# Kernel tuning notes

Measured on AMD Instinct MI355X. Metric: run time of the kernel, lower is better.

Reference implementation:

```python
import jax, jax.numpy as jnp
import numpy as np

D_MODEL = 1024
N_HEADS = 16
D_K = D_MODEL // N_HEADS
B, T = 2, 2048
EPS = 1e-6


def _phi(x):
    # elu(x) + 1
    return jax.nn.elu(x) + 1.0


def setup_inputs() -> dict:
    key = jax.random.key(0)
    ks = jax.random.split(key, 5)
    s = 1.0 / np.sqrt(D_MODEL)
    return {
        "x": jax.random.normal(ks[0], (B, T, D_MODEL), jnp.float32),
        "Wq": jax.random.normal(ks[1], (D_MODEL, D_MODEL), jnp.float32) * s,
        "bq": jnp.zeros((D_MODEL,), jnp.float32),
        "Wk": jax.random.normal(ks[2], (D_MODEL, D_MODEL), jnp.float32) * s,
        "bk": jnp.zeros((D_MODEL,), jnp.float32),
        "Wv": jax.random.normal(ks[3], (D_MODEL, D_MODEL), jnp.float32) * s,
        "bv": jnp.zeros((D_MODEL,), jnp.float32),
        "Wo": jax.random.normal(ks[4], (D_MODEL, D_MODEL), jnp.float32) * s,
        "bo": jnp.zeros((D_MODEL,), jnp.float32),
    }


def reference(x, Wq, bq, Wk, bk, Wv, bv, Wo, bo):
    Bv_, Tv_, _ = x.shape
    # projections (torch nn.Linear: x @ W.T + b), split heads -> [B, H, T, d_k]
    def proj(W, b):
        y = x @ W.T + b
        return y.reshape(Bv_, Tv_, N_HEADS, D_K).transpose(0, 2, 1, 3)

    q = _phi(proj(Wq, bq))
    k = _phi(proj(Wk, bk))
    v = proj(Wv, bv)

    # causal linear attention: running kv outer-product and k prefix sums
    kv = jnp.einsum("bhtd,bhte->bhtde", k, v)          # [B,H,T,d_k,d_k]
    kv = jnp.cumsum(kv, axis=2)
    k_cum = jnp.cumsum(k, axis=2)
    out = jnp.einsum("bhtd,bhtde->bhte", q, kv)        # [B,H,T,d_k]
    z = jnp.einsum("bhtd,bhtd->bht", q, k_cum)         # [B,H,T]
    out = out / (z[..., None] + EPS)

    out = out.transpose(0, 2, 1, 3).reshape(Bv_, Tv_, N_HEADS * D_K)
    return out @ Wo.T + bo
```

## Files before the change

kernel.cpp:

```cpp
#include <hip/hip_runtime.h>


typedef float  f32x4   __attribute__((ext_vector_type(4)));
typedef __bf16 bf16x8  __attribute__((ext_vector_type(8)));
typedef short  short8v __attribute__((ext_vector_type(8)));
typedef short  short4v __attribute__((ext_vector_type(4)));

static __device__ __forceinline__ short f2bf(float f) {
    unsigned u = __float_as_uint(f);
    u += 0x7FFFu + ((u >> 16) & 1u);
    return (short)(u >> 16);
}
static __device__ __forceinline__ float bf2f(short s) {
    return __uint_as_float(((unsigned)(unsigned short)s) << 16);
}
static __device__ __forceinline__ float phi(float x) {
    return x > 0.f ? x + 1.f : __expf(x);
}
static __device__ __forceinline__ void gl_lds16(const short* g, short* l) {
    __builtin_amdgcn_global_load_lds(
        (const __attribute__((address_space(1))) void*)g,
        (__attribute__((address_space(3))) void*)l, 16, 0, 0);
}

#define LDT 72
static __device__ __forceinline__ int swz(int row, int col) {
    return row * LDT + (col ^ (row & 56));
}

__global__ __launch_bounds__(256) void convert_bf16(
    const float* __restrict__ x,  const float* __restrict__ Wq,
    const float* __restrict__ Wk, const float* __restrict__ Wv,
    const float* __restrict__ Wo,
    short* __restrict__ xb,  short* __restrict__ Wqb,
    short* __restrict__ Wkb, short* __restrict__ Wvb, short* __restrict__ Wob)
{
    const int blk = blockIdx.x;
    const float* src; short* dst; size_t base;
    if (blk < 2048)      { src = x;  dst = xb;  base = (size_t)blk * 2048; }
    else if (blk < 2560) { src = Wq; dst = Wqb; base = (size_t)(blk - 2048) * 2048; }
    else if (blk < 3072) { src = Wk; dst = Wkb; base = (size_t)(blk - 2560) * 2048; }
    else if (blk < 3584) { src = Wv; dst = Wvb; base = (size_t)(blk - 3072) * 2048; }
    else                 { src = Wo; dst = Wob; base = (size_t)(blk - 3584) * 2048; }
    const size_t o = base + (size_t)threadIdx.x * 8;
    f32x4 v0 = *(const f32x4*)&src[o];
    f32x4 v1 = *(const f32x4*)&src[o + 4];
    short8v s;
#pragma unroll
    for (int m = 0; m < 4; ++m) { s[m] = f2bf(v0[m]); s[m + 4] = f2bf(v1[m]); }
    *(short8v*)&dst[o] = s;
}

__global__ __launch_bounds__(256) void gemm_qkv(
    const short* __restrict__ xb,
    const short* __restrict__ Wqb, const short* __restrict__ Wkb,
    const short* __restrict__ Wvb,
    const float* __restrict__ bq, const float* __restrict__ bk,
    const float* __restrict__ bv,
    short* __restrict__ Qb, short* __restrict__ Kb, short* __restrict__ Vb)
{
    __shared__ short As[2][128 * 32];
    __shared__ short Bs[2][128 * 32];
    const int tid = threadIdx.x;
    const int bm = blockIdx.x, bn = blockIdx.y;
    const int wsel = bn >> 3;
    const int n0 = (bn & 7) << 7;
    const short* __restrict__ W    = (wsel == 0) ? Wqb : (wsel == 1) ? Wkb : Wvb;
    const float* __restrict__ bias = (wsel == 0) ? bq  : (wsel == 1) ? bk  : bv;
    short* __restrict__ Ob         = (wsel == 0) ? Qb  : (wsel == 1) ? Kb  : Vb;
    const int m0 = bm << 7;
    const int wave = tid >> 6, lane = tid & 63;
    const int wm = (wave & 1) << 6, wn = (wave >> 1) << 6;
    const int l15 = lane & 15, quad = lane >> 4;

    const int ch0 = wave * 2, ch1 = ch0 + 1;
    const int lrow = lane >> 2;
    const int lcol = (((lane & 3) ^ ((lane >> 3) & 3)) << 3);
    const short* ga0 = xb + (size_t)(m0 + ch0 * 16 + lrow) * 1024 + lcol;
    const short* ga1 = xb + (size_t)(m0 + ch1 * 16 + lrow) * 1024 + lcol;
    const short* gb0 = W  + (size_t)(n0 + ch0 * 16 + lrow) * 1024 + lcol;
    const short* gb1 = W  + (size_t)(n0 + ch1 * 16 + lrow) * 1024 + lcol;
    short* la0[2] = { &As[0][ch0 * 512], &As[1][ch0 * 512] };
    short* la1[2] = { &As[0][ch1 * 512], &As[1][ch1 * 512] };
    short* lb0[2] = { &Bs[0][ch0 * 512], &Bs[1][ch0 * 512] };
    short* lb1[2] = { &Bs[0][ch1 * 512], &Bs[1][ch1 * 512] };

    const int rslot = (quad ^ ((l15 >> 1) & 3)) << 3;

#define QKV_STAGE(K, BUF)                    \
    do {                                     \
        gl_lds16(ga0 + (K), la0[BUF]);       \
        gl_lds16(ga1 + (K), la1[BUF]);       \
        gl_lds16(gb0 + (K), lb0[BUF]);       \
        gl_lds16(gb1 + (K), lb1[BUF]);       \
    } while (0)

#define QKV_COMPUTE(BUF)                                                              \
    do {                                                                              \
        bf16x8 a[4], b[4];                                                            \
        _Pragma("unroll")                                                             \
        for (int i = 0; i < 4; ++i)                                                   \
            a[i] = *(const bf16x8*)&As[BUF][(wm + i * 16 + l15) * 32 + rslot];        \
        _Pragma("unroll")                                                             \
        for (int j = 0; j < 4; ++j)                                                   \
            b[j] = *(const bf16x8*)&Bs[BUF][(wn + j * 16 + l15) * 32 + rslot];        \
        _Pragma("unroll")                                                             \
        for (int i = 0; i < 4; ++i)                                                   \
            _Pragma("unroll")                                                         \
            for (int j = 0; j < 4; ++j)                                               \
                acc[i][j] = __builtin_amdgcn_mfma_f32_16x16x32_bf16(a[i], b[j],       \
                                                                   acc[i][j], 0, 0, 0); \
    } while (0)

    f32x4 acc[4][4] = {};
    QKV_STAGE(0, 0);
    for (int k0 = 0; k0 < 1024; k0 += 64) {
        asm volatile("s_waitcnt vmcnt(0)" ::: "memory");
        __syncthreads();
        QKV_STAGE(k0 + 32, 1);
        QKV_COMPUTE(0);
        asm volatile("s_waitcnt vmcnt(0)" ::: "memory");
        __syncthreads();
        if (k0 + 64 < 1024) QKV_STAGE(k0 + 64, 0);
        QKV_COMPUTE(1);
    }
#undef QKV_STAGE
#undef QKV_COMPUTE

#pragma unroll
    for (int i = 0; i < 4; ++i)
#pragma unroll
        for (int j = 0; j < 4; ++j) {
            const int col = n0 + wn + j * 16 + l15;
            const int h = col >> 6, d = col & 63;
            const float bv_ = bias[col];
            const int row0 = m0 + wm + i * 16 + quad * 4;
            const int b = row0 >> 11, t0 = row0 & 2047;
            const size_t obase = ((size_t)(b * 16 + h) * 2048 + t0) * 64 + d;
#pragma unroll
            for (int r = 0; r < 4; ++r) {
                float v = acc[i][j][r] + bv_;
                if (wsel < 2) v = phi(v);
                Ob[obase + (size_t)r * 64] = f2bf(v);
            }
        }
}

__global__ __launch_bounds__(256) void chunk_sums(
    const short* __restrict__ Kb, const short* __restrict__ Vb,
    short* __restrict__ KVsum, float* __restrict__ ksum)
{
    __shared__ short KT[64 * LDT];
    __shared__ short VT[64 * LDT];
    __shared__ float pS[256];
    const int c = blockIdx.x, bh = blockIdx.y;
    const int tid = threadIdx.x;
    const int w = tid >> 6, lane = tid & 63, l15 = lane & 15, quad = lane >> 4;
    const size_t tilebase = ((size_t)bh * 2048 + c * 64) * 64;

#pragma unroll
    for (int p = 0; p < 2; ++p) {
        const int t = (tid >> 3) + p * 32;
        const int e0 = (tid & 7) << 3;
        const size_t g = tilebase + (size_t)t * 64 + e0;
        short8v kv = *(const short8v*)&Kb[g];
        short8v vv = *(const short8v*)&Vb[g];
#pragma unroll
        for (int jj = 0; jj < 8; ++jj) {
            KT[swz(e0 + jj, t)] = kv[jj];
            VT[swz(e0 + jj, t)] = vv[jj];
        }
    }
    __syncthreads();

    f32x4 acc[4] = {};
#pragma unroll
    for (int k0 = 0; k0 < 64; k0 += 32) {
        const int ra = w * 16 + l15;
        bf16x8 a = *(const bf16x8*)&KT[ra * LDT + ((k0 + quad * 8) ^ (ra & 56))];
#pragma unroll
        for (int tj = 0; tj < 4; ++tj) {
            const int rb = tj * 16 + l15;
            bf16x8 bfr = *(const bf16x8*)&VT[rb * LDT + ((k0 + quad * 8) ^ (rb & 56))];
            acc[tj] = __builtin_amdgcn_mfma_f32_16x16x32_bf16(a, bfr, acc[tj], 0, 0, 0);
        }
    }
    short* __restrict__ outp = KVsum + (((size_t)bh * 32) + c) * 4096;
#pragma unroll
    for (int tj = 0; tj < 4; ++tj)
#pragma unroll
        for (int r = 0; r < 4; ++r)
            outp[(w * 16 + quad * 4 + r) * 64 + tj * 16 + l15] = f2bf(acc[tj][r]);

    {
        const int d = tid & 63, part = tid >> 6;
        short8v k1 = *(const short8v*)&KT[d * LDT + ((part * 16) ^ (d & 56))];
        short8v k2 = *(const short8v*)&KT[d * LDT + ((part * 16 + 8) ^ (d & 56))];
        float s = 0.f;
#pragma unroll
        for (int m = 0; m < 8; ++m) s += bf2f(k1[m]) + bf2f(k2[m]);
        pS[part * 64 + d] = s;
    }
    __syncthreads();
    if (tid < 64)
        ksum[(((size_t)bh * 32) + c) * 64 + tid] =
            pS[tid] + pS[tid + 64] + pS[tid + 128] + pS[tid + 192];
}

__global__ __launch_bounds__(256) void scan_chunks(
    const short* __restrict__ KVsum, const float* __restrict__ ksum,
    short* __restrict__ KVpref, float* __restrict__ kpref)
{
    const int bh = blockIdx.y;
    const int o = blockIdx.x * 256 + threadIdx.x;
    const size_t base = (size_t)bh * 32 * 4096 + o;
    short v[32];
#pragma unroll
    for (int cc = 0; cc < 32; ++cc) v[cc] = KVsum[base + (size_t)cc * 4096];
    float run = 0.f;
#pragma unroll
    for (int cc = 0; cc < 32; ++cc) {
        KVpref[base + (size_t)cc * 4096] = f2bf(run);
        run += bf2f(v[cc]);
    }
    if (blockIdx.x == 0 && threadIdx.x < 64) {
        float vals[32];
        const size_t kb = (size_t)bh * 32 * 64 + threadIdx.x;
#pragma unroll
        for (int cc = 0; cc < 32; ++cc) vals[cc] = ksum[kb + (size_t)cc * 64];
        float r2 = 0.f;
#pragma unroll
        for (int cc = 0; cc < 32; ++cc) { kpref[kb + (size_t)cc * 64] = r2; r2 += vals[cc]; }
    }
}

__global__ __launch_bounds__(256) void attn_chunk(
    const short* __restrict__ Qb, const short* __restrict__ Kb,
    const short* __restrict__ Vb, const short* __restrict__ KVpref,
    const float* __restrict__ kpref, short* __restrict__ attnb)
{
    __shared__ short Qs[64 * LDT];
    __shared__ short KS[64 * LDT];
    __shared__ short VT[64 * LDT];
    __shared__ short KVT[64 * LDT];
    const int c = blockIdx.x, bh = blockIdx.y;
    const int b = bh >> 4, h = bh & 15;
    const int tid = threadIdx.x;
    const int w = tid >> 6, lane = tid & 63, l15 = lane & 15, quad = lane >> 4;
    const size_t tilebase = ((size_t)bh * 2048 + c * 64) * 64;
    const short* __restrict__ KVc = KVpref + (((size_t)bh * 32) + c) * 4096;

#pragma unroll
    for (int p = 0; p < 2; ++p) {
        const int t = (tid >> 3) + p * 32;
        const int e0 = (tid & 7) << 3;
        const size_t g = tilebase + (size_t)t * 64 + e0;
        *(short8v*)&Qs[t * LDT + e0] = *(const short8v*)&Qb[g];
        *(short8v*)&KS[t * LDT + e0] = *(const short8v*)&Kb[g];
        short8v vv = *(const short8v*)&Vb[g];
        short8v pv = *(const short8v*)&KVc[t * 64 + e0];
#pragma unroll
        for (int jj = 0; jj < 8; ++jj) {
            VT[swz(e0 + jj, t)]  = vv[jj];
            KVT[swz(e0 + jj, t)] = pv[jj];
        }
    }
    __syncthreads();

    f32x4 sacc[4] = {};
#pragma unroll
    for (int k0 = 0; k0 < 64; k0 += 32) {
        bf16x8 a = *(const bf16x8*)&Qs[(w * 16 + l15) * LDT + k0 + quad * 8];
#pragma unroll
        for (int tj = 0; tj < 4; ++tj) {
            bf16x8 bfr = *(const bf16x8*)&KS[(tj * 16 + l15) * LDT + k0 + quad * 8];
            sacc[tj] = __builtin_amdgcn_mfma_f32_16x16x32_bf16(a, bfr, sacc[tj], 0, 0, 0);
        }
    }

    f32x4 kp4 = *(const f32x4*)&kpref[(((size_t)bh * 32) + c) * 64 + l15 * 4];
    float zinv[4];
#pragma unroll
    for (int r = 0; r < 4; ++r) {
        const int i = w * 16 + quad * 4 + r;
        float p = 0.f;
#pragma unroll
        for (int tj = 0; tj < 4; ++tj)
            if (tj * 16 + l15 <= i) p += sacc[tj][r];
        short4v q4 = *(const short4v*)&Qs[i * LDT + l15 * 4];
#pragma unroll
        for (int m = 0; m < 4; ++m) p += bf2f(q4[m]) * kp4[m];
        p += __shfl_xor(p, 1);
        p += __shfl_xor(p, 2);
        p += __shfl_xor(p, 4);
        p += __shfl_xor(p, 8);
        zinv[r] = 1.f / (p + 1e-6f);
    }

    __syncthreads();
#pragma unroll
    for (int tj = 0; tj < 4; ++tj)
#pragma unroll
        for (int r = 0; r < 4; ++r) {
            const int i = w * 16 + quad * 4 + r;
            const int j = tj * 16 + l15;
            KS[i * LDT + j] = f2bf(j <= i ? sacc[tj][r] : 0.f);
        }

    f32x4 oacc[4] = {};
#pragma unroll
    for (int k0 = 0; k0 < 64; k0 += 32) {
        bf16x8 a1 = *(const bf16x8*)&KS[(w * 16 + l15) * LDT + k0 + quad * 8];
        bf16x8 a2 = *(const bf16x8*)&Qs[(w * 16 + l15) * LDT + k0 + quad * 8];
#pragma unroll
        for (int tj = 0; tj < 4; ++tj) {
            const int rb = tj * 16 + l15;
            bf16x8 b1 = *(const bf16x8*)&VT[rb * LDT + ((k0 + quad * 8) ^ (rb & 56))];
            bf16x8 b2 = *(const bf16x8*)&KVT[rb * LDT + ((k0 + quad * 8) ^ (rb & 56))];
            oacc[tj] = __builtin_amdgcn_mfma_f32_16x16x32_bf16(a1, b1, oacc[tj], 0, 0, 0);
            oacc[tj] = __builtin_amdgcn_mfma_f32_16x16x32_bf16(a2, b2, oacc[tj], 0, 0, 0);
        }
    }
    const size_t arowbase = (size_t)b * 2048 + c * 64;
#pragma unroll
    for (int tj = 0; tj < 4; ++tj)
#pragma unroll
        for (int r = 0; r < 4; ++r) {
            const int i = w * 16 + quad * 4 + r;
            const int e = tj * 16 + l15;
            attnb[(arowbase + i) * 1024 + h * 64 + e] = f2bf(oacc[tj][r] * zinv[r]);
        }
}

__global__ __launch_bounds__(256) void gemm_out(
    const short* __restrict__ attnb, const short* __restrict__ Wob,
    const float* __restrict__ bo, float* __restrict__ outp)
{
    __shared__ short As[2][128 * 32];
    __shared__ short Bs[2][64 * 32];
    const int tid = threadIdx.x;
    const int bm = blockIdx.x, bn = blockIdx.y;
    const int m0 = bm << 7, n0 = bn << 6;
    const int wave = tid >> 6, lane = tid & 63;
    const int wm = (wave & 1) << 6, wn = (wave >> 1) << 5;
    const int l15 = lane & 15, quad = lane >> 4;

    const int lrow = lane >> 2;
    const int lcol = (((lane & 3) ^ ((lane >> 3) & 3)) << 3);
    const short* gp[3]; short* lp[2][3];
#pragma unroll
    for (int cc = 0; cc < 3; ++cc) {
        const int ch = wave * 3 + cc;
        if (ch < 8) {
            gp[cc] = attnb + (size_t)(m0 + ch * 16 + lrow) * 1024 + lcol;
            lp[0][cc] = &As[0][ch * 512];
            lp[1][cc] = &As[1][ch * 512];
        } else {
            gp[cc] = Wob + (size_t)(n0 + (ch - 8) * 16 + lrow) * 1024 + lcol;
            lp[0][cc] = &Bs[0][(ch - 8) * 512];
            lp[1][cc] = &Bs[1][(ch - 8) * 512];
        }
    }
    const int rslot = (quad ^ ((l15 >> 1) & 3)) << 3;

#define OUT_STAGE(K, BUF)                     \
    do {                                      \
        gl_lds16(gp[0] + (K), lp[BUF][0]);    \
        gl_lds16(gp[1] + (K), lp[BUF][1]);    \
        gl_lds16(gp[2] + (K), lp[BUF][2]);    \
    } while (0)

#define OUT_COMPUTE(BUF)                                                              \
    do {                                                                              \
        bf16x8 a[4], b[2];                                                            \
        _Pragma("unroll")                                                             \
        for (int i = 0; i < 4; ++i)                                                   \
            a[i] = *(const bf16x8*)&As[BUF][(wm + i * 16 + l15) * 32 + rslot];        \
        _Pragma("unroll")                                                             \
        for (int j = 0; j < 2; ++j)                                                   \
            b[j] = *(const bf16x8*)&Bs[BUF][(wn + j * 16 + l15) * 32 + rslot];        \
        _Pragma("unroll")                                                             \
        for (int i = 0; i < 4; ++i)                                                   \
            _Pragma("unroll")                                                         \
            for (int j = 0; j < 2; ++j)                                               \
                acc[i][j] = __builtin_amdgcn_mfma_f32_16x16x32_bf16(a[i], b[j],       \
                                                                   acc[i][j], 0, 0, 0); \
    } while (0)

    f32x4 acc[4][2] = {};
    OUT_STAGE(0, 0);
    for (int k0 = 0; k0 < 1024; k0 += 64) {
        asm volatile("s_waitcnt vmcnt(0)" ::: "memory");
        __syncthreads();
        OUT_STAGE(k0 + 32, 1);
        OUT_COMPUTE(0);
        asm volatile("s_waitcnt vmcnt(0)" ::: "memory");
        __syncthreads();
        if (k0 + 64 < 1024) OUT_STAGE(k0 + 64, 0);
        OUT_COMPUTE(1);
    }
#undef OUT_STAGE
#undef OUT_COMPUTE

#pragma unroll
    for (int i = 0; i < 4; ++i)
#pragma unroll
        for (int j = 0; j < 2; ++j) {
            const int col = n0 + wn + j * 16 + l15;
            const float bv_ = bo[col];
#pragma unroll
            for (int r = 0; r < 4; ++r) {
                const int row = m0 + wm + i * 16 + quad * 4 + r;
                outp[(size_t)row * 1024 + col] = acc[i][j][r] + bv_;
            }
        }
}

extern "C" void kernel_launch(void* const* d_in, const int* in_sizes, int n_in,
                              void* d_out, int out_size, void* d_ws, size_t ws_size,
                              hipStream_t stream)
{
    const float* x  = (const float*)d_in[0];
    const float* Wq = (const float*)d_in[1];
    const float* bq = (const float*)d_in[2];
    const float* Wk = (const float*)d_in[3];
    const float* bk = (const float*)d_in[4];
    const float* Wv = (const float*)d_in[5];
    const float* bv = (const float*)d_in[6];
    const float* Wo = (const float*)d_in[7];
    const float* bo = (const float*)d_in[8];

    char* ws = (char*)d_ws;
    short* xb     = (short*)(ws + 0);
    short* Wqb    = (short*)(ws + 8388608);
    short* Wkb    = (short*)(ws + 10485760);
    short* Wvb    = (short*)(ws + 12582912);
    short* Wob    = (short*)(ws + 14680064);
    short* Qb     = (short*)(ws + 16777216);
    short* Kb     = (short*)(ws + 25165824);
    short* Vb     = (short*)(ws + 33554432);
    short* KVsum  = (short*)(ws + 41943040);
    short* KVpref = (short*)(ws + 50331648);
    short* attnb  = (short*)(ws + 58720256);
    float* ksum   = (float*)(ws + 67108864);
    float* kpref  = (float*)(ws + 67371008);
    float* outp   = (float*)d_out;

    convert_bf16<<<4096, 256, 0, stream>>>(x, Wq, Wk, Wv, Wo, xb, Wqb, Wkb, Wvb, Wob);
    gemm_qkv   <<<dim3(32, 24), 256, 0, stream>>>(xb, Wqb, Wkb, Wvb, bq, bk, bv, Qb, Kb, Vb);
    chunk_sums <<<dim3(32, 32), 256, 0, stream>>>(Kb, Vb, KVsum, ksum);
    scan_chunks<<<dim3(16, 32), 256, 0, stream>>>(KVsum, ksum, KVpref, kpref);
    attn_chunk <<<dim3(32, 32), 256, 0, stream>>>(Qb, Kb, Vb, KVpref, kpref, attnb);
    gemm_out   <<<dim3(32, 16), 256, 0, stream>>>(attnb, Wob, bo, outp);
}
```

Baseline: 160.7 us.

## Fuse all six stages into one persistent kernel with grid barriers

```diff
diff --git a/kernel.cpp b/kernel.cpp
--- a/kernel.cpp
+++ b/kernel.cpp
@@ -28,64 +28,99 @@
     return row * LDT + (col ^ (row & 56));
 }
 
-__global__ __launch_bounds__(256) void convert_bf16(
-    const float* __restrict__ x,  const float* __restrict__ Wq,
-    const float* __restrict__ Wk, const float* __restrict__ Wv,
-    const float* __restrict__ Wo,
-    short* __restrict__ xb,  short* __restrict__ Wqb,
-    short* __restrict__ Wkb, short* __restrict__ Wvb, short* __restrict__ Wob)
+#define NBLK 768
+
+static __device__ __forceinline__ void gbar(unsigned* bar) {
+    __syncthreads();
+    if (threadIdx.x == 0) {
+        unsigned* arrive = bar;
+        unsigned* gen    = bar + 32;
+        __builtin_amdgcn_fence(__ATOMIC_RELEASE, "agent");
+        unsigned g = __hip_atomic_load(gen, __ATOMIC_RELAXED, __HIP_MEMORY_SCOPE_AGENT);
+        unsigned a = __hip_atomic_fetch_add(arrive, 1u, __ATOMIC_RELAXED, __HIP_MEMORY_SCOPE_AGENT);
+        if (a == NBLK - 1u) {
+            __hip_atomic_store(arrive, 0u, __ATOMIC_RELAXED, __HIP_MEMORY_SCOPE_AGENT);
+            __hip_atomic_store(gen, g + 1u, __ATOMIC_RELEASE, __HIP_MEMORY_SCOPE_AGENT);
+        } else {
+            while (__hip_atomic_load(gen, __ATOMIC_RELAXED, __HIP_MEMORY_SCOPE_AGENT) == g)
+                __builtin_amdgcn_s_sleep(8);
+        }
+        __builtin_amdgcn_fence(__ATOMIC_ACQUIRE, "agent");
+    }
+    __syncthreads();
+}
+
+__global__ __launch_bounds__(256, 3) void mega(
+    const float* __restrict__ x,
+    const float* __restrict__ Wq, const float* __restrict__ bq,
+    const float* __restrict__ Wk, const float* __restrict__ bk,
+    const float* __restrict__ Wv, const float* __restrict__ bv,
+    const float* __restrict__ Wo, const float* __restrict__ bo,
+    char* __restrict__ ws, float* __restrict__ outp)
 {
-    const int blk = blockIdx.x;
-    const float* src; short* dst; size_t base;
-    if (blk < 2048)      { src = x;  dst = xb;  base = (size_t)blk * 2048; }
-    else if (blk < 2560) { src = Wq; dst = Wqb; base = (size_t)(blk - 2048) * 2048; }
-    else if (blk < 3072) { src = Wk; dst = Wkb; base = (size_t)(blk - 2560) * 2048; }
-    else if (blk < 3584) { src = Wv; dst = Wvb; base = (size_t)(blk - 3072) * 2048; }
-    else                 { src = Wo; dst = Wob; base = (size_t)(blk - 3584) * 2048; }
-    const size_t o = base + (size_t)threadIdx.x * 8;
-    f32x4 v0 = *(const f32x4*)&src[o];
-    f32x4 v1 = *(const f32x4*)&src[o + 4];
-    short8v s;
-#pragma unroll
-    for (int m = 0; m < 4; ++m) { s[m] = f2bf(v0[m]); s[m + 4] = f2bf(v1[m]); }
-    *(short8v*)&dst[o] = s;
-}
-
-__global__ __launch_bounds__(256) void gemm_qkv(
-    const short* __restrict__ xb,
-    const short* __restrict__ Wqb, const short* __restrict__ Wkb,
-    const short* __restrict__ Wvb,
-    const float* __restrict__ bq, const float* __restrict__ bk,
-    const float* __restrict__ bv,
-    short* __restrict__ Qb, short* __restrict__ Kb, short* __restrict__ Vb)
-{
-    __shared__ short As[2][128 * 32];
-    __shared__ short Bs[2][128 * 32];
+    __shared__ __align__(16) char smem[36864];
+
+    const int bid = blockIdx.x;
     const int tid = threadIdx.x;
-    const int bm = blockIdx.x, bn = blockIdx.y;
-    const int wsel = bn >> 3;
-    const int n0 = (bn & 7) << 7;
-    const short* __restrict__ W    = (wsel == 0) ? Wqb : (wsel == 1) ? Wkb : Wvb;
-    const float* __restrict__ bias = (wsel == 0) ? bq  : (wsel == 1) ? bk  : bv;
-    short* __restrict__ Ob         = (wsel == 0) ? Qb  : (wsel == 1) ? Kb  : Vb;
-    const int m0 = bm << 7;
     const int wave = tid >> 6, lane = tid & 63;
-    const int wm = (wave & 1) << 6, wn = (wave >> 1) << 6;
     const int l15 = lane & 15, quad = lane >> 4;
 
-    const int ch0 = wave * 2, ch1 = ch0 + 1;
-    const int lrow = lane >> 2;
-    const int lcol = (((lane & 3) ^ ((lane >> 3) & 3)) << 3);
-    const short* ga0 = xb + (size_t)(m0 + ch0 * 16 + lrow) * 1024 + lcol;
-    const short* ga1 = xb + (size_t)(m0 + ch1 * 16 + lrow) * 1024 + lcol;
-    const short* gb0 = W  + (size_t)(n0 + ch0 * 16 + lrow) * 1024 + lcol;
-    const short* gb1 = W  + (size_t)(n0 + ch1 * 16 + lrow) * 1024 + lcol;
-    short* la0[2] = { &As[0][ch0 * 512], &As[1][ch0 * 512] };
-    short* la1[2] = { &As[0][ch1 * 512], &As[1][ch1 * 512] };
-    short* lb0[2] = { &Bs[0][ch0 * 512], &Bs[1][ch0 * 512] };
-    short* lb1[2] = { &Bs[0][ch1 * 512], &Bs[1][ch1 * 512] };
-
-    const int rslot = (quad ^ ((l15 >> 1) & 3)) << 3;
+    short* xb     = (short*)(ws + 0);
+    short* Wqb    = (short*)(ws + 8388608);
+    short* Wkb    = (short*)(ws + 10485760);
+    short* Wvb    = (short*)(ws + 12582912);
+    short* Wob    = (short*)(ws + 14680064);
+    short* Qb     = (short*)(ws + 16777216);
+    short* Kb     = (short*)(ws + 25165824);
+    short* Vb     = (short*)(ws + 33554432);
+    short* KVsum  = (short*)(ws + 41943040);
+    short* KVpref = (short*)(ws + 50331648);
+    short* attnb  = (short*)(ws + 58720256);
+    float* ksum   = (float*)(ws + 67108864);
+    float* kpref  = (float*)(ws + 67371008);
+    unsigned* bar = (unsigned*)(ws + 68157440);
+
+    for (int u = bid; u < 4096; u += NBLK) {
+        const float* src; short* dst; size_t base;
+        if (u < 2048)      { src = x;  dst = xb;  base = (size_t)u * 2048; }
+        else if (u < 2560) { src = Wq; dst = Wqb; base = (size_t)(u - 2048) * 2048; }
+        else if (u < 3072) { src = Wk; dst = Wkb; base = (size_t)(u - 2560) * 2048; }
+        else if (u < 3584) { src = Wv; dst = Wvb; base = (size_t)(u - 3072) * 2048; }
+        else               { src = Wo; dst = Wob; base = (size_t)(u - 3584) * 2048; }
+        const size_t o = base + (size_t)tid * 8;
+        f32x4 v0 = *(const f32x4*)&src[o];
+        f32x4 v1 = *(const f32x4*)&src[o + 4];
+        short8v s;
+#pragma unroll
+        for (int m = 0; m < 4; ++m) { s[m] = f2bf(v0[m]); s[m + 4] = f2bf(v1[m]); }
+        *(short8v*)&dst[o] = s;
+    }
+    gbar(bar);
+
+    {
+        short* Asb[2] = { (short*)smem,        (short*)smem + 4096 };
+        short* Bsb[2] = { (short*)smem + 8192, (short*)smem + 12288 };
+        const int bm = bid & 31, bn = bid >> 5;
+        const int wsel = bn >> 3;
+        const int n0 = (bn & 7) << 7;
+        const short* __restrict__ W    = (wsel == 0) ? Wqb : (wsel == 1) ? Wkb : Wvb;
+        const float* __restrict__ bias = (wsel == 0) ? bq  : (wsel == 1) ? bk  : bv;
+        short* __restrict__ Ob         = (wsel == 0) ? Qb  : (wsel == 1) ? Kb  : Vb;
+        const int m0 = bm << 7;
+        const int wm = (wave & 1) << 6, wn = (wave >> 1) << 6;
+
+        const int ch0 = wave * 2, ch1 = ch0 + 1;
+        const int lrow = lane >> 2;
+        const int lcol = (((lane & 3) ^ ((lane >> 3) & 3)) << 3);
+        const short* ga0 = xb + (size_t)(m0 + ch0 * 16 + lrow) * 1024 + lcol;
+        const short* ga1 = xb + (size_t)(m0 + ch1 * 16 + lrow) * 1024 + lcol;
+        const short* gb0 = W  + (size_t)(n0 + ch0 * 16 + lrow) * 1024 + lcol;
+        const short* gb1 = W  + (size_t)(n0 + ch1 * 16 + lrow) * 1024 + lcol;
+        short* la0[2] = { Asb[0] + ch0 * 512, Asb[1] + ch0 * 512 };
+        short* la1[2] = { Asb[0] + ch1 * 512, Asb[1] + ch1 * 512 };
+        short* lb0[2] = { Bsb[0] + ch0 * 512, Bsb[1] + ch0 * 512 };
+        short* lb1[2] = { Bsb[0] + ch1 * 512, Bsb[1] + ch1 * 512 };
+        const int rslot = (quad ^ ((l15 >> 1) & 3)) << 3;
 
 #define QKV_STAGE(K, BUF)                    \
     do {                                     \
@@ -94,16 +129,15 @@
         gl_lds16(gb0 + (K), lb0[BUF]);       \
         gl_lds16(gb1 + (K), lb1[BUF]);       \
     } while (0)
-
 #define QKV_COMPUTE(BUF)                                                              \
     do {                                                                              \
         bf16x8 a[4], b[4];                                                            \
         _Pragma("unroll")                                                             \
         for (int i = 0; i < 4; ++i)                                                   \
-            a[i] = *(const bf16x8*)&As[BUF][(wm + i * 16 + l15) * 32 + rslot];        \
+            a[i] = *(const bf16x8*)&Asb[BUF][(wm + i * 16 + l15) * 32 + rslot];       \
         _Pragma("unroll")                                                             \
         for (int j = 0; j < 4; ++j)                                                   \
-            b[j] = *(const bf16x8*)&Bs[BUF][(wn + j * 16 + l15) * 32 + rslot];        \
+            b[j] = *(const bf16x8*)&Bsb[BUF][(wn + j * 16 + l15) * 32 + rslot];       \
         _Pragma("unroll")                                                             \
         for (int i = 0; i < 4; ++i)                                                   \
             _Pragma("unroll")                                                         \
@@ -112,256 +146,247 @@
                                                                    acc[i][j], 0, 0, 0); \
     } while (0)
 
-    f32x4 acc[4][4] = {};
-    QKV_STAGE(0, 0);
-    for (int k0 = 0; k0 < 1024; k0 += 64) {
-        asm volatile("s_waitcnt vmcnt(0)" ::: "memory");
-        __syncthreads();
-        QKV_STAGE(k0 + 32, 1);
-        QKV_COMPUTE(0);
-        asm volatile("s_waitcnt vmcnt(0)" ::: "memory");
-        __syncthreads();
-        if (k0 + 64 < 1024) QKV_STAGE(k0 + 64, 0);
-        QKV_COMPUTE(1);
-    }
+        f32x4 acc[4][4] = {};
+        QKV_STAGE(0, 0);
+        for (int k0 = 0; k0 < 1024; k0 += 64) {
+            asm volatile("s_waitcnt vmcnt(0)" ::: "memory");
+            __syncthreads();
+            QKV_STAGE(k0 + 32, 1);
+            QKV_COMPUTE(0);
+            asm volatile("s_waitcnt vmcnt(0)" ::: "memory");
+            __syncthreads();
+            if (k0 + 64 < 1024) QKV_STAGE(k0 + 64, 0);
+            QKV_COMPUTE(1);
+        }
 #undef QKV_STAGE
 #undef QKV_COMPUTE
 
 #pragma unroll
-    for (int i = 0; i < 4; ++i)
-#pragma unroll
-        for (int j = 0; j < 4; ++j) {
-            const int col = n0 + wn + j * 16 + l15;
-            const int h = col >> 6, d = col & 63;
-            const float bv_ = bias[col];
-            const int row0 = m0 + wm + i * 16 + quad * 4;
-            const int b = row0 >> 11, t0 = row0 & 2047;
-            const size_t obase = ((size_t)(b * 16 + h) * 2048 + t0) * 64 + d;
+        for (int i = 0; i < 4; ++i)
+#pragma unroll
+            for (int j = 0; j < 4; ++j) {
+                const int col = n0 + wn + j * 16 + l15;
+                const int h = col >> 6, d = col & 63;
+                const float bv_ = bias[col];
+                const int row0 = m0 + wm + i * 16 + quad * 4;
+                const int b = row0 >> 11, t0 = row0 & 2047;
+                const size_t obase = ((size_t)(b * 16 + h) * 2048 + t0) * 64 + d;
+#pragma unroll
+                for (int r = 0; r < 4; ++r) {
+                    float v = acc[i][j][r] + bv_;
+                    if (wsel < 2) v = phi(v);
+                    Ob[obase + (size_t)r * 64] = f2bf(v);
+                }
+            }
+    }
+    gbar(bar);
+
+    {
+        short* KT = (short*)smem;
+        short* VT = KT + 4608;
+        float* pS = (float*)(VT + 4608);
+        const int w = wave;
+        for (int tidx = bid; tidx < 1024; tidx += NBLK) {
+            const int c = tidx & 31, bh = tidx >> 5;
+            const size_t tilebase = ((size_t)bh * 2048 + c * 64) * 64;
+            __syncthreads();
+#pragma unroll
+            for (int p = 0; p < 2; ++p) {
+                const int t = (tid >> 3) + p * 32;
+                const int e0 = (tid & 7) << 3;
+                const size_t g = tilebase + (size_t)t * 64 + e0;
+                short8v kv = *(const short8v*)&Kb[g];
+                short8v vv = *(const short8v*)&Vb[g];
+#pragma unroll
+                for (int jj = 0; jj < 8; ++jj) {
+                    KT[swz(e0 + jj, t)] = kv[jj];
+                    VT[swz(e0 + jj, t)] = vv[jj];
+                }
+            }
+            __syncthreads();
+
+            f32x4 acc[4] = {};
+#pragma unroll
+            for (int k0 = 0; k0 < 64; k0 += 32) {
+                const int ra = w * 16 + l15;
+                bf16x8 a = *(const bf16x8*)&KT[ra * LDT + ((k0 + quad * 8) ^ (ra & 56))];
+#pragma unroll
+                for (int tj = 0; tj < 4; ++tj) {
+                    const int rb = tj * 16 + l15;
+                    bf16x8 bfr = *(const bf16x8*)&VT[rb * LDT + ((k0 + quad * 8) ^ (rb & 56))];
+                    acc[tj] = __builtin_amdgcn_mfma_f32_16x16x32_bf16(a, bfr, acc[tj], 0, 0, 0);
+                }
+            }
+            short* __restrict__ op = KVsum + (((size_t)bh * 32) + c) * 4096;
+#pragma unroll
+            for (int tj = 0; tj < 4; ++tj)
+#pragma unroll
+                for (int r = 0; r < 4; ++r)
+                    op[(w * 16 + quad * 4 + r) * 64 + tj * 16 + l15] = f2bf(acc[tj][r]);
+
+            {
+                const int d = tid & 63, part = tid >> 6;
+                short8v k1 = *(const short8v*)&KT[d * LDT + ((part * 16) ^ (d & 56))];
+                short8v k2 = *(const short8v*)&KT[d * LDT + ((part * 16 + 8) ^ (d & 56))];
+                float s = 0.f;
+#pragma unroll
+                for (int m = 0; m < 8; ++m) s += bf2f(k1[m]) + bf2f(k2[m]);
+                pS[part * 64 + d] = s;
+            }
+            __syncthreads();
+            if (tid < 64)
+                ksum[(((size_t)bh * 32) + c) * 64 + tid] =
+                    pS[tid] + pS[tid + 64] + pS[tid + 128] + pS[tid + 192];
+        }
+    }
+    gbar(bar);
+
+    if (bid < 512) {
+        const int bx = bid & 15, bh = bid >> 4;
+        const int o = bx * 256 + tid;
+        const size_t base = (size_t)bh * 32 * 4096 + o;
+        short v[32];
+#pragma unroll
+        for (int cc = 0; cc < 32; ++cc) v[cc] = KVsum[base + (size_t)cc * 4096];
+        float run = 0.f;
+#pragma unroll
+        for (int cc = 0; cc < 32; ++cc) {
+            KVpref[base + (size_t)cc * 4096] = f2bf(run);
+            run += bf2f(v[cc]);
+        }
+        if (bx == 0 && tid < 64) {
+            float vals[32];
+            const size_t kb = (size_t)bh * 32 * 64 + tid;
+#pragma unroll
+            for (int cc = 0; cc < 32; ++cc) vals[cc] = ksum[kb + (size_t)cc * 64];
+            float r2 = 0.f;
+#pragma unroll
+            for (int cc = 0; cc < 32; ++cc) { kpref[kb + (size_t)cc * 64] = r2; r2 += vals[cc]; }
+        }
+    }
+    gbar(bar);
+
+    {
+        short* Qs  = (short*)smem;
+        short* KS  = Qs + 4608;
+        short* VTa = KS + 4608;
+        short* KVT = VTa + 4608;
+        const int w = wave;
+        for (int tidx = bid; tidx < 1024; tidx += NBLK) {
+            const int c = tidx & 31, bh = tidx >> 5;
+            const int b = bh >> 4, h = bh & 15;
+            const size_t tilebase = ((size_t)bh * 2048 + c * 64) * 64;
+            const short* __restrict__ KVc = KVpref + (((size_t)bh * 32) + c) * 4096;
+
+            __syncthreads();
+#pragma unroll
+            for (int p = 0; p < 2; ++p) {
+                const int t = (tid >> 3) + p * 32;
+                const int e0 = (tid & 7) << 3;
+                const size_t g = tilebase + (size_t)t * 64 + e0;
+                *(short8v*)&Qs[t * LDT + e0] = *(const short8v*)&Qb[g];
+                *(short8v*)&KS[t * LDT + e0] = *(const short8v*)&Kb[g];
+                short8v vv = *(const short8v*)&Vb[g];
+                short8v pv = *(const short8v*)&KVc[t * 64 + e0];
+#pragma unroll
+                for (int jj = 0; jj < 8; ++jj) {
+                    VTa[swz(e0 + jj, t)] = vv[jj];
+                    KVT[swz(e0 + jj, t)] = pv[jj];
+                }
+            }
+            __syncthreads();
+
+            f32x4 sacc[4] = {};
+#pragma unroll
+            for (int k0 = 0; k0 < 64; k0 += 32) {
+                bf16x8 a = *(const bf16x8*)&Qs[(w * 16 + l15) * LDT + k0 + quad * 8];
+#pragma unroll
+                for (int tj = 0; tj < 4; ++tj) {
+                    bf16x8 bfr = *(const bf16x8*)&KS[(tj * 16 + l15) * LDT + k0 + quad * 8];
+                    sacc[tj] = __builtin_amdgcn_mfma_f32_16x16x32_bf16(a, bfr, sacc[tj], 0, 0, 0);
+                }
+            }
+
+            f32x4 kp4 = *(const f32x4*)&kpref[(((size_t)bh * 32) + c) * 64 + l15 * 4];
+            float zinv[4];
 #pragma unroll
             for (int r = 0; r < 4; ++r) {
-                float v = acc[i][j][r] + bv_;
-                if (wsel < 2) v = phi(v);
-                Ob[obase + (size_t)r * 64] = f2bf(v);
-            }
-        }
-}
-
-__global__ __launch_bounds__(256) void chunk_sums(
-    const short* __restrict__ Kb, const short* __restrict__ Vb,
-    short* __restrict__ KVsum, float* __restrict__ ksum)
-{
-    __shared__ short KT[64 * LDT];
-    __shared__ short VT[64 * LDT];
-    __shared__ float pS[256];
-    const int c = blockIdx.x, bh = blockIdx.y;
-    const int tid = threadIdx.x;
-    const int w = tid >> 6, lane = tid & 63, l15 = lane & 15, quad = lane >> 4;
-    const size_t tilebase = ((size_t)bh * 2048 + c * 64) * 64;
-
-#pragma unroll
-    for (int p = 0; p < 2; ++p) {
-        const int t = (tid >> 3) + p * 32;
-        const int e0 = (tid & 7) << 3;
-        const size_t g = tilebase + (size_t)t * 64 + e0;
-        short8v kv = *(const short8v*)&Kb[g];
-        short8v vv = *(const short8v*)&Vb[g];
-#pragma unroll
-        for (int jj = 0; jj < 8; ++jj) {
-            KT[swz(e0 + jj, t)] = kv[jj];
-            VT[swz(e0 + jj, t)] = vv[jj];
-        }
-    }
-    __syncthreads();
-
-    f32x4 acc[4] = {};
-#pragma unroll
-    for (int k0 = 0; k0 < 64; k0 += 32) {
-        const int ra = w * 16 + l15;
-        bf16x8 a = *(const bf16x8*)&KT[ra * LDT + ((k0 + quad * 8) ^ (ra & 56))];
-#pragma unroll
-        for (int tj = 0; tj < 4; ++tj) {
-            const int rb = tj * 16 + l15;
-            bf16x8 bfr = *(const bf16x8*)&VT[rb * LDT + ((k0 + quad * 8) ^ (rb & 56))];
-            acc[tj] = __builtin_amdgcn_mfma_f32_16x16x32_bf16(a, bfr, acc[tj], 0, 0, 0);
-        }
-    }
-    short* __restrict__ outp = KVsum + (((size_t)bh * 32) + c) * 4096;
-#pragma unroll
-    for (int tj = 0; tj < 4; ++tj)
-#pragma unroll
-        for (int r = 0; r < 4; ++r)
-            outp[(w * 16 + quad * 4 + r) * 64 + tj * 16 + l15] = f2bf(acc[tj][r]);
-
-    {
-        const int d = tid & 63, part = tid >> 6;
-        short8v k1 = *(const short8v*)&KT[d * LDT + ((part * 16) ^ (d & 56))];
-        short8v k2 = *(const short8v*)&KT[d * LDT + ((part * 16 + 8) ^ (d & 56))];
-        float s = 0.f;
-#pragma unroll
-        for (int m = 0; m < 8; ++m) s += bf2f(k1[m]) + bf2f(k2[m]);
-        pS[part * 64 + d] = s;
-    }
-    __syncthreads();
-    if (tid < 64)
-        ksum[(((size_t)bh * 32) + c) * 64 + tid] =
-            pS[tid] + pS[tid + 64] + pS[tid + 128] + pS[tid + 192];
-}
-
-__global__ __launch_bounds__(256) void scan_chunks(
-    const short* __restrict__ KVsum, const float* __restrict__ ksum,
-    short* __restrict__ KVpref, float* __restrict__ kpref)
-{
-    const int bh = blockIdx.y;
-    const int o = blockIdx.x * 256 + threadIdx.x;
-    const size_t base = (size_t)bh * 32 * 4096 + o;
-    short v[32];
-#pragma unroll
-    for (int cc = 0; cc < 32; ++cc) v[cc] = KVsum[base + (size_t)cc * 4096];
-    float run = 0.f;
-#pragma unroll
-    for (int cc = 0; cc < 32; ++cc) {
-        KVpref[base + (size_t)cc * 4096] = f2bf(run);
-        run += bf2f(v[cc]);
-    }
-    if (blockIdx.x == 0 && threadIdx.x < 64) {
-        float vals[32];
-        const size_t kb = (size_t)bh * 32 * 64 + threadIdx.x;
-#pragma unroll
-        for (int cc = 0; cc < 32; ++cc) vals[cc] = ksum[kb + (size_t)cc * 64];
-        float r2 = 0.f;
-#pragma unroll
-        for (int cc = 0; cc < 32; ++cc) { kpref[kb + (size_t)cc * 64] = r2; r2 += vals[cc]; }
-    }
-}
-
-__global__ __launch_bounds__(256) void attn_chunk(
-    const short* __restrict__ Qb, const short* __restrict__ Kb,
-    const short* __restrict__ Vb, const short* __restrict__ KVpref,
-    const float* __restrict__ kpref, short* __restrict__ attnb)
-{
-    __shared__ short Qs[64 * LDT];
-    __shared__ short KS[64 * LDT];
-    __shared__ short VT[64 * LDT];
-    __shared__ short KVT[64 * LDT];
-    const int c = blockIdx.x, bh = blockIdx.y;
-    const int b = bh >> 4, h = bh & 15;
-    const int tid = threadIdx.x;
-    const int w = tid >> 6, lane = tid & 63, l15 = lane & 15, quad = lane >> 4;
-    const size_t tilebase = ((size_t)bh * 2048 + c * 64) * 64;
-    const short* __restrict__ KVc = KVpref + (((size_t)bh * 32) + c) * 4096;
-
-#pragma unroll
-    for (int p = 0; p < 2; ++p) {
-        const int t = (tid >> 3) + p * 32;
-        const int e0 = (tid & 7) << 3;
-        const size_t g = tilebase + (size_t)t * 64 + e0;
-        *(short8v*)&Qs[t * LDT + e0] = *(const short8v*)&Qb[g];
-        *(short8v*)&KS[t * LDT + e0] = *(const short8v*)&Kb[g];
-        short8v vv = *(const short8v*)&Vb[g];
-        short8v pv = *(const short8v*)&KVc[t * 64 + e0];
-#pragma unroll
-        for (int jj = 0; jj < 8; ++jj) {
-            VT[swz(e0 + jj, t)]  = vv[jj];
-            KVT[swz(e0 + jj, t)] = pv[jj];
-        }
-    }
-    __syncthreads();
-
-    f32x4 sacc[4] = {};
-#pragma unroll
-    for (int k0 = 0; k0 < 64; k0 += 32) {
-        bf16x8 a = *(const bf16x8*)&Qs[(w * 16 + l15) * LDT + k0 + quad * 8];
-#pragma unroll
-        for (int tj = 0; tj < 4; ++tj) {
-            bf16x8 bfr = *(const bf16x8*)&KS[(tj * 16 + l15) * LDT + k0 + quad * 8];
-            sacc[tj] = __builtin_amdgcn_mfma_f32_16x16x32_bf16(a, bfr, sacc[tj], 0, 0, 0);
-        }
-    }
-
-    f32x4 kp4 = *(const f32x4*)&kpref[(((size_t)bh * 32) + c) * 64 + l15 * 4];
-    float zinv[4];
-#pragma unroll
-    for (int r = 0; r < 4; ++r) {
-        const int i = w * 16 + quad * 4 + r;
-        float p = 0.f;
-#pragma unroll
-        for (int tj = 0; tj < 4; ++tj)
-            if (tj * 16 + l15 <= i) p += sacc[tj][r];
-        short4v q4 = *(const short4v*)&Qs[i * LDT + l15 * 4];
-#pragma unroll
-        for (int m = 0; m < 4; ++m) p += bf2f(q4[m]) * kp4[m];
-        p += __shfl_xor(p, 1);
-        p += __shfl_xor(p, 2);
-        p += __shfl_xor(p, 4);
-        p += __shfl_xor(p, 8);
-        zinv[r] = 1.f / (p + 1e-6f);
-    }
-
-    __syncthreads();
-#pragma unroll
-    for (int tj = 0; tj < 4; ++tj)
-#pragma unroll
-        for (int r = 0; r < 4; ++r) {
-            const int i = w * 16 + quad * 4 + r;
-            const int j = tj * 16 + l15;
-            KS[i * LDT + j] = f2bf(j <= i ? sacc[tj][r] : 0.f);
-        }
-
-    f32x4 oacc[4] = {};
-#pragma unroll
-    for (int k0 = 0; k0 < 64; k0 += 32) {
-        bf16x8 a1 = *(const bf16x8*)&KS[(w * 16 + l15) * LDT + k0 + quad * 8];
-        bf16x8 a2 = *(const bf16x8*)&Qs[(w * 16 + l15) * LDT + k0 + quad * 8];
-#pragma unroll
-        for (int tj = 0; tj < 4; ++tj) {
-            const int rb = tj * 16 + l15;
-            bf16x8 b1 = *(const bf16x8*)&VT[rb * LDT + ((k0 + quad * 8) ^ (rb & 56))];
-            bf16x8 b2 = *(const bf16x8*)&KVT[rb * LDT + ((k0 + quad * 8) ^ (rb & 56))];
-            oacc[tj] = __builtin_amdgcn_mfma_f32_16x16x32_bf16(a1, b1, oacc[tj], 0, 0, 0);
-            oacc[tj] = __builtin_amdgcn_mfma_f32_16x16x32_bf16(a2, b2, oacc[tj], 0, 0, 0);
-        }
-    }
-    const size_t arowbase = (size_t)b * 2048 + c * 64;
-#pragma unroll
-    for (int tj = 0; tj < 4; ++tj)
-#pragma unroll
-        for (int r = 0; r < 4; ++r) {
-            const int i = w * 16 + quad * 4 + r;
-            const int e = tj * 16 + l15;
-            attnb[(arowbase + i) * 1024 + h * 64 + e] = f2bf(oacc[tj][r] * zinv[r]);
-        }
-}
-
-__global__ __launch_bounds__(256) void gemm_out(
-    const short* __restrict__ attnb, const short* __restrict__ Wob,
-    const float* __restrict__ bo, float* __restrict__ outp)
-{
-    __shared__ short As[2][128 * 32];
-    __shared__ short Bs[2][64 * 32];
-    const int tid = threadIdx.x;
-    const int bm = blockIdx.x, bn = blockIdx.y;
-    const int m0 = bm << 7, n0 = bn << 6;
-    const int wave = tid >> 6, lane = tid & 63;
-    const int wm = (wave & 1) << 6, wn = (wave >> 1) << 5;
-    const int l15 = lane & 15, quad = lane >> 4;
-
-    const int lrow = lane >> 2;
-    const int lcol = (((lane & 3) ^ ((lane >> 3) & 3)) << 3);
-    const short* gp[3]; short* lp[2][3];
-#pragma unroll
-    for (int cc = 0; cc < 3; ++cc) {
-        const int ch = wave * 3 + cc;
-        if (ch < 8) {
-            gp[cc] = attnb + (size_t)(m0 + ch * 16 + lrow) * 1024 + lcol;
-            lp[0][cc] = &As[0][ch * 512];
-            lp[1][cc] = &As[1][ch * 512];
-        } else {
-            gp[cc] = Wob + (size_t)(n0 + (ch - 8) * 16 + lrow) * 1024 + lcol;
-            lp[0][cc] = &Bs[0][(ch - 8) * 512];
-            lp[1][cc] = &Bs[1][(ch - 8) * 512];
-        }
-    }
-    const int rslot = (quad ^ ((l15 >> 1) & 3)) << 3;
+                const int i = w * 16 + quad * 4 + r;
+                float p = 0.f;
+#pragma unroll
+                for (int tj = 0; tj < 4; ++tj)
+                    if (tj * 16 + l15 <= i) p += sacc[tj][r];
+                short4v q4 = *(const short4v*)&Qs[i * LDT + l15 * 4];
+#pragma unroll
+                for (int m = 0; m < 4; ++m) p += bf2f(q4[m]) * kp4[m];
+                p += __shfl_xor(p, 1);
+                p += __shfl_xor(p, 2);
+                p += __shfl_xor(p, 4);
+                p += __shfl_xor(p, 8);
+                zinv[r] = 1.f / (p + 1e-6f);
+            }
+
+            __syncthreads();
+#pragma unroll
+            for (int tj = 0; tj < 4; ++tj)
+#pragma unroll
+                for (int r = 0; r < 4; ++r) {
+                    const int i = w * 16 + quad * 4 + r;
+                    const int j = tj * 16 + l15;
+                    KS[i * LDT + j] = f2bf(j <= i ? sacc[tj][r] : 0.f);
+                }
+
+            f32x4 oacc[4] = {};
+#pragma unroll
+            for (int k0 = 0; k0 < 64; k0 += 32) {
+                bf16x8 a1 = *(const bf16x8*)&KS[(w * 16 + l15) * LDT + k0 + quad * 8];
+                bf16x8 a2 = *(const bf16x8*)&Qs[(w * 16 + l15) * LDT + k0 + quad * 8];
+#pragma unroll
+                for (int tj = 0; tj < 4; ++tj) {
+                    const int rb = tj * 16 + l15;
+                    bf16x8 b1 = *(const bf16x8*)&VTa[rb * LDT + ((k0 + quad * 8) ^ (rb & 56))];
+                    bf16x8 b2 = *(const bf16x8*)&KVT[rb * LDT + ((k0 + quad * 8) ^ (rb & 56))];
+                    oacc[tj] = __builtin_amdgcn_mfma_f32_16x16x32_bf16(a1, b1, oacc[tj], 0, 0, 0);
+                    oacc[tj] = __builtin_amdgcn_mfma_f32_16x16x32_bf16(a2, b2, oacc[tj], 0, 0, 0);
+                }
+            }
+            const size_t arowbase = (size_t)b * 2048 + c * 64;
+#pragma unroll
+            for (int tj = 0; tj < 4; ++tj)
+#pragma unroll
+                for (int r = 0; r < 4; ++r) {
+                    const int i = w * 16 + quad * 4 + r;
+                    const int e = tj * 16 + l15;
+                    attnb[(arowbase + i) * 1024 + h * 64 + e] = f2bf(oacc[tj][r] * zinv[r]);
+                }
+        }
+    }
+    gbar(bar);
+
+    if (bid < 512) {
+        short* Aob[2] = { (short*)smem,        (short*)smem + 4096 };
+        short* Bob[2] = { (short*)smem + 8192, (short*)smem + 10240 };
+        const int bm = bid & 31, bn = bid >> 5;
+        const int m0 = bm << 7, n0 = bn << 6;
+        const int wm = (wave & 1) << 6, wn = (wave >> 1) << 5;
+
+        const int lrow = lane >> 2;
+        const int lcol = (((lane & 3) ^ ((lane >> 3) & 3)) << 3);
+        const short* gp[3]; short* lp[2][3];
+#pragma unroll
+        for (int cc = 0; cc < 3; ++cc) {
+            const int ch = wave * 3 + cc;
+            if (ch < 8) {
+                gp[cc] = attnb + (size_t)(m0 + ch * 16 + lrow) * 1024 + lcol;
+                lp[0][cc] = Aob[0] + ch * 512;
+                lp[1][cc] = Aob[1] + ch * 512;
+            } else {
+                gp[cc] = Wob + (size_t)(n0 + (ch - 8) * 16 + lrow) * 1024 + lcol;
+                lp[0][cc] = Bob[0] + (ch - 8) * 512;
+                lp[1][cc] = Bob[1] + (ch - 8) * 512;
+            }
+        }
+        const int rslot = (quad ^ ((l15 >> 1) & 3)) << 3;
 
 #define OUT_STAGE(K, BUF)                     \
     do {                                      \
@@ -369,16 +394,15 @@
         gl_lds16(gp[1] + (K), lp[BUF][1]);    \
         gl_lds16(gp[2] + (K), lp[BUF][2]);    \
     } while (0)
-
 #define OUT_COMPUTE(BUF)                                                              \
     do {                                                                              \
         bf16x8 a[4], b[2];                                                            \
         _Pragma("unroll")                                                             \
         for (int i = 0; i < 4; ++i)                                                   \
-            a[i] = *(const bf16x8*)&As[BUF][(wm + i * 16 + l15) * 32 + rslot];        \
+            a[i] = *(const bf16x8*)&Aob[BUF][(wm + i * 16 + l15) * 32 + rslot];       \
         _Pragma("unroll")                                                             \
         for (int j = 0; j < 2; ++j)                                                   \
-            b[j] = *(const bf16x8*)&Bs[BUF][(wn + j * 16 + l15) * 32 + rslot];        \
+            b[j] = *(const bf16x8*)&Bob[BUF][(wn + j * 16 + l15) * 32 + rslot];       \
         _Pragma("unroll")                                                             \
         for (int i = 0; i < 4; ++i)                                                   \
             _Pragma("unroll")                                                         \
@@ -387,33 +411,34 @@
                                                                    acc[i][j], 0, 0, 0); \
     } while (0)
 
-    f32x4 acc[4][2] = {};
-    OUT_STAGE(0, 0);
-    for (int k0 = 0; k0 < 1024; k0 += 64) {
-        asm volatile("s_waitcnt vmcnt(0)" ::: "memory");
-        __syncthreads();
-        OUT_STAGE(k0 + 32, 1);
-        OUT_COMPUTE(0);
-        asm volatile("s_waitcnt vmcnt(0)" ::: "memory");
-        __syncthreads();
-        if (k0 + 64 < 1024) OUT_STAGE(k0 + 64, 0);
-        OUT_COMPUTE(1);
-    }
+        f32x4 acc[4][2] = {};
+        OUT_STAGE(0, 0);
+        for (int k0 = 0; k0 < 1024; k0 += 64) {
+            asm volatile("s_waitcnt vmcnt(0)" ::: "memory");
+            __syncthreads();
+            OUT_STAGE(k0 + 32, 1);
+            OUT_COMPUTE(0);
+            asm volatile("s_waitcnt vmcnt(0)" ::: "memory");
+            __syncthreads();
+            if (k0 + 64 < 1024) OUT_STAGE(k0 + 64, 0);
+            OUT_COMPUTE(1);
+        }
 #undef OUT_STAGE
 #undef OUT_COMPUTE
 
 #pragma unroll
-    for (int i = 0; i < 4; ++i)
-#pragma unroll
-        for (int j = 0; j < 2; ++j) {
-            const int col = n0 + wn + j * 16 + l15;
-            const float bv_ = bo[col];
-#pragma unroll
-            for (int r = 0; r < 4; ++r) {
-                const int row = m0 + wm + i * 16 + quad * 4 + r;
-                outp[(size_t)row * 1024 + col] = acc[i][j][r] + bv_;
-            }
-        }
+        for (int i = 0; i < 4; ++i)
+#pragma unroll
+            for (int j = 0; j < 2; ++j) {
+                const int col = n0 + wn + j * 16 + l15;
+                const float bv_ = bo[col];
+#pragma unroll
+                for (int r = 0; r < 4; ++r) {
+                    const int row = m0 + wm + i * 16 + quad * 4 + r;
+                    outp[(size_t)row * 1024 + col] = acc[i][j][r] + bv_;
+                }
+            }
+    }
 }
 
 extern "C" void kernel_launch(void* const* d_in, const int* in_sizes, int n_in,
@@ -429,27 +454,11 @@
     const float* bv = (const float*)d_in[6];
     const float* Wo = (const float*)d_in[7];
     const float* bo = (const float*)d_in[8];
-
     char* ws = (char*)d_ws;
-    short* xb     = (short*)(ws + 0);
-    short* Wqb    = (short*)(ws + 8388608);
-    short* Wkb    = (short*)(ws + 10485760);
-    short* Wvb    = (short*)(ws + 12582912);
-    short* Wob    = (short*)(ws + 14680064);
-    short* Qb     = (short*)(ws + 16777216);
-    short* Kb     = (short*)(ws + 25165824);
-    short* Vb     = (short*)(ws + 33554432);
-    short* KVsum  = (short*)(ws + 41943040);
-    short* KVpref = (short*)(ws + 50331648);
-    short* attnb  = (short*)(ws + 58720256);
-    float* ksum   = (float*)(ws + 67108864);
-    float* kpref  = (float*)(ws + 67371008);
-    float* outp   = (float*)d_out;
-
-    convert_bf16<<<4096, 256, 0, stream>>>(x, Wq, Wk, Wv, Wo, xb, Wqb, Wkb, Wvb, Wob);
-    gemm_qkv   <<<dim3(32, 24), 256, 0, stream>>>(xb, Wqb, Wkb, Wvb, bq, bk, bv, Qb, Kb, Vb);
-    chunk_sums <<<dim3(32, 32), 256, 0, stream>>>(Kb, Vb, KVsum, ksum);
-    scan_chunks<<<dim3(16, 32), 256, 0, stream>>>(KVsum, ksum, KVpref, kpref);
-    attn_chunk <<<dim3(32, 32), 256, 0, stream>>>(Qb, Kb, Vb, KVpref, kpref, attnb);
-    gemm_out   <<<dim3(32, 16), 256, 0, stream>>>(attnb, Wob, bo, outp);
-}
+    float* outp = (float*)d_out;
+
+    hipMemsetAsync(ws + 68157440, 0, 256, stream);
+
+    mega<<<dim3(NBLK), dim3(256), 0, stream>>>(
+        x, Wq, bq, Wk, bk, Wv, bv, Wo, bo, ws, outp);
+}
```

Result: slower. 289.9 us (+80.4%).

## Triple-buffer LDS in QKV and output GEMMs with one barrier per k-step

Applied to the files above, without the earlier changes.

```diff
diff --git a/kernel.cpp b/kernel.cpp
--- a/kernel.cpp
+++ b/kernel.cpp
@@ -59,8 +59,8 @@
     const float* __restrict__ bv,
     short* __restrict__ Qb, short* __restrict__ Kb, short* __restrict__ Vb)
 {
-    __shared__ short As[2][128 * 32];
-    __shared__ short Bs[2][128 * 32];
+    __shared__ short As[3][128 * 32];
+    __shared__ short Bs[3][128 * 32];
     const int tid = threadIdx.x;
     const int bm = blockIdx.x, bn = blockIdx.y;
     const int wsel = bn >> 3;
@@ -80,19 +80,15 @@
     const short* ga1 = xb + (size_t)(m0 + ch1 * 16 + lrow) * 1024 + lcol;
     const short* gb0 = W  + (size_t)(n0 + ch0 * 16 + lrow) * 1024 + lcol;
     const short* gb1 = W  + (size_t)(n0 + ch1 * 16 + lrow) * 1024 + lcol;
-    short* la0[2] = { &As[0][ch0 * 512], &As[1][ch0 * 512] };
-    short* la1[2] = { &As[0][ch1 * 512], &As[1][ch1 * 512] };
-    short* lb0[2] = { &Bs[0][ch0 * 512], &Bs[1][ch0 * 512] };
-    short* lb1[2] = { &Bs[0][ch1 * 512], &Bs[1][ch1 * 512] };
-
+    const int lo0 = ch0 * 512, lo1 = ch1 * 512;
     const int rslot = (quad ^ ((l15 >> 1) & 3)) << 3;
 
-#define QKV_STAGE(K, BUF)                    \
-    do {                                     \
-        gl_lds16(ga0 + (K), la0[BUF]);       \
-        gl_lds16(ga1 + (K), la1[BUF]);       \
-        gl_lds16(gb0 + (K), lb0[BUF]);       \
-        gl_lds16(gb1 + (K), lb1[BUF]);       \
+#define QKV_STAGE(K, BUF)                        \
+    do {                                         \
+        gl_lds16(ga0 + (K), &As[BUF][lo0]);      \
+        gl_lds16(ga1 + (K), &As[BUF][lo1]);      \
+        gl_lds16(gb0 + (K), &Bs[BUF][lo0]);      \
+        gl_lds16(gb1 + (K), &Bs[BUF][lo1]);      \
     } while (0)
 
 #define QKV_COMPUTE(BUF)                                                              \
@@ -112,18 +108,33 @@
                                                                    acc[i][j], 0, 0, 0); \
     } while (0)
 
+#define QKV_STEP(T, RB, SB)                                   \
+    do {                                                      \
+        asm volatile("s_waitcnt vmcnt(4)" ::: "memory");      \
+        __builtin_amdgcn_s_barrier();                         \
+        __builtin_amdgcn_sched_barrier(0);                    \
+        QKV_STAGE(((T) + 2) * 32, SB);                        \
+        QKV_COMPUTE(RB);                                      \
+    } while (0)
+
     f32x4 acc[4][4] = {};
     QKV_STAGE(0, 0);
-    for (int k0 = 0; k0 < 1024; k0 += 64) {
-        asm volatile("s_waitcnt vmcnt(0)" ::: "memory");
-        __syncthreads();
-        QKV_STAGE(k0 + 32, 1);
-        QKV_COMPUTE(0);
-        asm volatile("s_waitcnt vmcnt(0)" ::: "memory");
-        __syncthreads();
-        if (k0 + 64 < 1024) QKV_STAGE(k0 + 64, 0);
-        QKV_COMPUTE(1);
-    }
+    QKV_STAGE(32, 1);
+    for (int u = 0; u < 10; ++u) {
+        const int t = u * 3;
+        QKV_STEP(t + 0, 0, 2);
+        QKV_STEP(t + 1, 1, 0);
+        QKV_STEP(t + 2, 2, 1);
+    }
+    asm volatile("s_waitcnt vmcnt(4)" ::: "memory");
+    __builtin_amdgcn_s_barrier();
+    __builtin_amdgcn_sched_barrier(0);
+    QKV_COMPUTE(0);
+    asm volatile("s_waitcnt vmcnt(0)" ::: "memory");
+    __builtin_amdgcn_s_barrier();
+    __builtin_amdgcn_sched_barrier(0);
+    QKV_COMPUTE(1);
+#undef QKV_STEP
 #undef QKV_STAGE
 #undef QKV_COMPUTE
 
@@ -336,8 +347,8 @@
     const short* __restrict__ attnb, const short* __restrict__ Wob,
     const float* __restrict__ bo, float* __restrict__ outp)
 {
-    __shared__ short As[2][128 * 32];
-    __shared__ short Bs[2][64 * 32];
+    __shared__ short As[3][128 * 32];
+    __shared__ short Bs[3][64 * 32];
     const int tid = threadIdx.x;
     const int bm = blockIdx.x, bn = blockIdx.y;
     const int m0 = bm << 7, n0 = bn << 6;
@@ -347,27 +358,26 @@
 
     const int lrow = lane >> 2;
     const int lcol = (((lane & 3) ^ ((lane >> 3) & 3)) << 3);
-    const short* gp[3]; short* lp[2][3];
+    const short* gp[3]; int lof[3]; bool isA[3];
 #pragma unroll
     for (int cc = 0; cc < 3; ++cc) {
         const int ch = wave * 3 + cc;
         if (ch < 8) {
             gp[cc] = attnb + (size_t)(m0 + ch * 16 + lrow) * 1024 + lcol;
-            lp[0][cc] = &As[0][ch * 512];
-            lp[1][cc] = &As[1][ch * 512];
+            lof[cc] = ch * 512;  isA[cc] = true;
         } else {
             gp[cc] = Wob + (size_t)(n0 + (ch - 8) * 16 + lrow) * 1024 + lcol;
-            lp[0][cc] = &Bs[0][(ch - 8) * 512];
-            lp[1][cc] = &Bs[1][(ch - 8) * 512];
+            lof[cc] = (ch - 8) * 512;  isA[cc] = false;
         }
     }
     const int rslot = (quad ^ ((l15 >> 1) & 3)) << 3;
 
-#define OUT_STAGE(K, BUF)                     \
-    do {                                      \
-        gl_lds16(gp[0] + (K), lp[BUF][0]);    \
-        gl_lds16(gp[1] + (K), lp[BUF][1]);    \
-        gl_lds16(gp[2] + (K), lp[BUF][2]);    \
+#define OUT_STAGE(K, BUF)                                                   \
+    do {                                                                    \
+        _Pragma("unroll")                                                   \
+        for (int cc = 0; cc < 3; ++cc)                                      \
+            gl_lds16(gp[cc] + (K), (isA[cc] ? &As[BUF][lof[cc]]             \
+                                            : &Bs[BUF][lof[cc]]));          \
     } while (0)
 
 #define OUT_COMPUTE(BUF)                                                              \
@@ -387,18 +397,33 @@
                                                                    acc[i][j], 0, 0, 0); \
     } while (0)
 
+#define OUT_STEP(T, RB, SB)                                   \
+    do {                                                      \
+        asm volatile("s_waitcnt vmcnt(3)" ::: "memory");      \
+        __builtin_amdgcn_s_barrier();                         \
+        __builtin_amdgcn_sched_barrier(0);                    \
+        OUT_STAGE(((T) + 2) * 32, SB);                        \
+        OUT_COMPUTE(RB);                                      \
+    } while (0)
+
     f32x4 acc[4][2] = {};
     OUT_STAGE(0, 0);
-    for (int k0 = 0; k0 < 1024; k0 += 64) {
-        asm volatile("s_waitcnt vmcnt(0)" ::: "memory");
-        __syncthreads();
-        OUT_STAGE(k0 + 32, 1);
-        OUT_COMPUTE(0);
-        asm volatile("s_waitcnt vmcnt(0)" ::: "memory");
-        __syncthreads();
-        if (k0 + 64 < 1024) OUT_STAGE(k0 + 64, 0);
-        OUT_COMPUTE(1);
-    }
+    OUT_STAGE(32, 1);
+    for (int u = 0; u < 10; ++u) {
+        const int t = u * 3;
+        OUT_STEP(t + 0, 0, 2);
+        OUT_STEP(t + 1, 1, 0);
+        OUT_STEP(t + 2, 2, 1);
+    }
+    asm volatile("s_waitcnt vmcnt(3)" ::: "memory");
+    __builtin_amdgcn_s_barrier();
+    __builtin_amdgcn_sched_barrier(0);
+    OUT_COMPUTE(0);
+    asm volatile("s_waitcnt vmcnt(0)" ::: "memory");
+    __builtin_amdgcn_s_barrier();
+    __builtin_amdgcn_sched_barrier(0);
+    OUT_COMPUTE(1);
+#undef OUT_STEP
 #undef OUT_STAGE
 #undef OUT_COMPUTE
 
```

Measured after the change: 179.2 us. 11.5% more time.
